# Performance work log

Hardware: AMD Instinct MI355X
Metric: run time of the kernel (lower is better)

## Reference

```python
import jax, jax.numpy as jnp
import numpy as np

H = 128          # hidden_dim
N_LAYERS = 3
N_GRAPHS = 256
LN_EPS = 1e-5


def setup_inputs() -> dict:
    key = jax.random.key(0)
    ks = jax.random.split(key, 12)
    N, E = 100000, 600000
    x = jax.random.normal(ks[0], (N, 66), dtype=jnp.float32)
    edge_index = jax.random.randint(ks[1], (2, E), 0, N, dtype=jnp.int32)
    edge_attr = jax.random.normal(ks[2], (E, 6), dtype=jnp.float32)
    batch = jnp.sort(jax.random.randint(ks[3], (N,), 0, N_GRAPHS, dtype=jnp.int32))
    # params (stored as [in, out] so y = x @ W + b)
    def lin(k, fan_in, fan_out):
        s = 1.0 / np.sqrt(fan_in)
        kw, kb = jax.random.split(k)
        return (jax.random.uniform(kw, (fan_in, fan_out), jnp.float32, -s, s),
                jax.random.uniform(kb, (fan_out,), jnp.float32, -s, s))
    w_node, b_node = lin(ks[4], 66, H)
    w_edge, b_edge = lin(ks[5], 6, H)
    mp_ws, mp_bs = [], []
    for i in range(N_LAYERS):
        w, b = lin(ks[6 + i], 3 * H, H)
        mp_ws.append(w); mp_bs.append(b)
    w_out, b_out = lin(ks[9], H, H)
    return {
        "x": x, "edge_index": edge_index, "edge_attr": edge_attr, "batch": batch,
        "w_node": w_node, "b_node": b_node, "w_edge": w_edge, "b_edge": b_edge,
        "mp_w": jnp.stack(mp_ws), "mp_b": jnp.stack(mp_bs),
        "ln_g": jnp.ones((H,), jnp.float32), "ln_b": jnp.zeros((H,), jnp.float32),
        "w_out": w_out, "b_out": b_out,
    }


def _layer_norm(h, g, b):
    mu = h.mean(-1, keepdims=True)
    var = ((h - mu) ** 2).mean(-1, keepdims=True)
    return (h - mu) * jax.lax.rsqrt(var + LN_EPS) * g + b


def reference(x, edge_index, edge_attr, batch, w_node, b_node, w_edge, b_edge,
              mp_w, mp_b, ln_g, ln_b, w_out, b_out):
    h = x @ w_node + b_node                      # [N, H]
    ef = edge_attr @ w_edge + b_edge             # [E, H]
    src, dst = edge_index[0], edge_index[1]
    for i in range(N_LAYERS):
        W = mp_w[i]                               # [3H, H], split to avoid concat
        Ws, Wd, We = W[:H], W[H:2 * H], W[2 * H:]
        # per-edge message = Linear(concat(h[src], h[dst], ef)); original takes a
        # GLOBAL mean over all edges -> single [H] vector broadcast to all nodes
        msgs = h[src] @ Ws + h[dst] @ Wd + ef @ We   # [E, H]
        mean_msg = msgs.mean(axis=0) + mp_b[i]       # [H]
        h = h + mean_msg
        h = jax.nn.relu(_layer_norm(h, ln_g, ln_b))
        # dropout is identity in eval mode
    counts = jax.ops.segment_sum(jnp.ones((h.shape[0],), h.dtype), batch,
                                 num_segments=N_GRAPHS)
    pooled = jax.ops.segment_sum(h, batch, num_segments=N_GRAPHS)
    pooled = pooled / jnp.maximum(counts, 1.0)[:, None]   # global_mean_pool
    return pooled @ w_out + b_out                 # [N_GRAPHS, H]
```

## Files before the change

### kernel.cpp

```cpp
#include <hip/hip_runtime.h>

#define HDIM 128
#define XDIM 66
#define EDIM 6
#define NGRAPHS 256
#define LN_EPS 1e-5f
#define T0ROWS 64

#define HBINS 25600
#define HR 4
#define HB 32
#define CBINS (HR * HBINS)
#define NBX 1024

__global__ __launch_bounds__(256) void k_hist_part(const int* __restrict__ ei,
        float* __restrict__ part, int E) {
    __shared__ float lh[HBINS];
    int b = blockIdx.x;
    int s = b & (HB - 1);
    int r = (b / HB) & (HR - 1);
    int a = b / (HB * HR);
    int t = threadIdx.x;
    for (int i = t; i < HBINS; i += 256) lh[i] = 0.f;
    __syncthreads();
    const int* src = ei + (size_t)a * E;
    int chunk = (((E + HB - 1) / HB) + 3) & ~3;
    int lo = s * chunk;
    int hi = min(E, lo + chunk);
    int base = r * HBINS;
    if ((E & 3) == 0) {
        for (int i = lo + t * 4; i < hi; i += 256 * 4) {
            if (i + 4 <= hi) {
                int4 v = *(const int4*)(src + i);
                unsigned u0 = (unsigned)(v.x - base);
                unsigned u1 = (unsigned)(v.y - base);
                unsigned u2 = (unsigned)(v.z - base);
                unsigned u3 = (unsigned)(v.w - base);
                if (u0 < HBINS) atomicAdd(&lh[u0], 1.0f);
                if (u1 < HBINS) atomicAdd(&lh[u1], 1.0f);
                if (u2 < HBINS) atomicAdd(&lh[u2], 1.0f);
                if (u3 < HBINS) atomicAdd(&lh[u3], 1.0f);
            } else {
                for (int j = i; j < hi; ++j) {
                    unsigned u = (unsigned)(src[j] - base);
                    if (u < HBINS) atomicAdd(&lh[u], 1.0f);
                }
            }
        }
    } else {
        for (int i = lo + t; i < hi; i += 256) {
            unsigned u = (unsigned)(src[i] - base);
            if (u < HBINS) atomicAdd(&lh[u], 1.0f);
        }
    }
    __syncthreads();
    float* dst = part + (size_t)b * HBINS;
    for (int i = t; i < HBINS / 4; i += 256)
        ((float4*)dst)[i] = ((const float4*)lh)[i];
}

__global__ __launch_bounds__(256) void k_hist_red(const float* __restrict__ part,
        float* __restrict__ c_src, float* __restrict__ c_dst) {
    int n = blockIdx.x * 256 + threadIdx.x;
    if (n >= CBINS) return;
    int r = n / HBINS, off = n - r * HBINS;
    const float* p0 = part + ((size_t)(0 * HR + r) * HB) * HBINS + off;
    const float* p1 = part + ((size_t)(1 * HR + r) * HB) * HBINS + off;
    float s0 = 0.f, s1 = 0.f;
#pragma unroll 8
    for (int s = 0; s < HB; ++s) {
        s0 += p0[(size_t)s * HBINS];
        s1 += p1[(size_t)s * HBINS];
    }
    c_src[n] = s0;
    c_dst[n] = s1;
}

__global__ __launch_bounds__(256) void k_edgesum(const float* __restrict__ ea,
                                                 float* __restrict__ sum_attr, int E) {
    int nchunk = E >> 1;
    float a0 = 0, a1 = 0, a2 = 0, a3 = 0, a4 = 0, a5 = 0;
    for (int c = blockIdx.x * blockDim.x + threadIdx.x; c < nchunk;
         c += gridDim.x * blockDim.x) {
        const float4* p = (const float4*)(ea + (size_t)c * 12);
        float4 v0 = p[0], v1 = p[1], v2 = p[2];
        a0 += v0.x + v1.z;  a1 += v0.y + v1.w;  a2 += v0.z + v2.x;
        a3 += v0.w + v2.y;  a4 += v1.x + v2.z;  a5 += v1.y + v2.w;
    }
#pragma unroll
    for (int m = 32; m; m >>= 1) {
        a0 += __shfl_xor(a0, m); a1 += __shfl_xor(a1, m); a2 += __shfl_xor(a2, m);
        a3 += __shfl_xor(a3, m); a4 += __shfl_xor(a4, m); a5 += __shfl_xor(a5, m);
    }
    __shared__ float sbuf[4][6];
    int lane = threadIdx.x & 63, w = threadIdx.x >> 6;
    if (lane == 0) {
        sbuf[w][0] = a0; sbuf[w][1] = a1; sbuf[w][2] = a2;
        sbuf[w][3] = a3; sbuf[w][4] = a4; sbuf[w][5] = a5;
    }
    __syncthreads();
    if (threadIdx.x < 6) {
        float s = sbuf[0][threadIdx.x] + sbuf[1][threadIdx.x] +
                  sbuf[2][threadIdx.x] + sbuf[3][threadIdx.x];
        atomicAdd(&sum_attr[threadIdx.x], s);
    }
    if (blockIdx.x == 0 && threadIdx.x < 6 && (E & 1))
        atomicAdd(&sum_attr[threadIdx.x], ea[(size_t)(E - 1) * 6 + threadIdx.x]);
}

__global__ __launch_bounds__(256) void k_xsum(const float* __restrict__ x,
        const float* __restrict__ c_src, const float* __restrict__ c_dst,
        float* __restrict__ xpart, int N) {
    int lane = threadIdx.x & 63, w = threadIdx.x >> 6;
    int wid = blockIdx.x * 4 + w, nw = gridDim.x * 4;
    float as0 = 0, ad0 = 0, as1 = 0, ad1 = 0;
    int Q = N >> 2;
    for (int q = wid; q < Q; q += nw) {
        int n = q * 4;
        const float* xr = x + (size_t)n * XDIM;
        float x0 = xr[lane];
        float x1 = xr[XDIM + lane];
        float x2 = xr[2 * XDIM + lane];
        float x3 = xr[3 * XDIM + lane];
        float4 cs = *(const float4*)(c_src + n);
        float4 cd = *(const float4*)(c_dst + n);
        as0 = fmaf(cs.x, x0, as0); as0 = fmaf(cs.y, x1, as0);
        as0 = fmaf(cs.z, x2, as0); as0 = fmaf(cs.w, x3, as0);
        ad0 = fmaf(cd.x, x0, ad0); ad0 = fmaf(cd.y, x1, ad0);
        ad0 = fmaf(cd.z, x2, ad0); ad0 = fmaf(cd.w, x3, ad0);
        if (lane < 2) {
            float e0 = xr[64 + lane];
            float e1 = xr[XDIM + 64 + lane];
            float e2 = xr[2 * XDIM + 64 + lane];
            float e3 = xr[3 * XDIM + 64 + lane];
            as1 = fmaf(cs.x, e0, as1); as1 = fmaf(cs.y, e1, as1);
            as1 = fmaf(cs.z, e2, as1); as1 = fmaf(cs.w, e3, as1);
            ad1 = fmaf(cd.x, e0, ad1); ad1 = fmaf(cd.y, e1, ad1);
            ad1 = fmaf(cd.z, e2, ad1); ad1 = fmaf(cd.w, e3, ad1);
        }
    }
    if (wid == 0) {
        for (int n = Q * 4; n < N; ++n) {
            const float* xr = x + (size_t)n * XDIM;
            float cs = c_src[n], cd = c_dst[n];
            float xv = xr[lane];
            as0 = fmaf(cs, xv, as0);
            ad0 = fmaf(cd, xv, ad0);
            if (lane < 2) {
                float xe = xr[64 + lane];
                as1 = fmaf(cs, xe, as1);
                ad1 = fmaf(cd, xe, ad1);
            }
        }
    }
    __shared__ float redS[4][XDIM], redD[4][XDIM];
    redS[w][lane] = as0;  redD[w][lane] = ad0;
    if (lane < 2) { redS[w][64 + lane] = as1;  redD[w][64 + lane] = ad1; }
    __syncthreads();
    int t = threadIdx.x;
    float* xp = xpart + (size_t)blockIdx.x * 136;
    if (t < XDIM) {
        xp[t]        = redS[0][t] + redS[1][t] + redS[2][t] + redS[3][t];
        xp[XDIM + t] = redD[0][t] + redD[1][t] + redD[2][t] + redD[3][t];
    }
}

__global__ __launch_bounds__(64) void k_xred(const float* __restrict__ xpart,
                                             float* __restrict__ xs, int nb) {
    int e = blockIdx.x;
    int lane = threadIdx.x;
    float s = 0.f;
    for (int b = lane; b < nb; b += 64)
        s += xpart[(size_t)b * 136 + e];
#pragma unroll
    for (int m = 32; m; m >>= 1) s += __shfl_xor(s, m);
    if (lane == 0) xs[e] = s;
}

template <int FIRST>
__global__ __launch_bounds__(256) void k_mm(const float* __restrict__ sv,
        const float* __restrict__ sum_attr, const float* __restrict__ w_edge,
        const float* __restrict__ b_edge, const float* __restrict__ W,
        const float* __restrict__ mpb, float* __restrict__ mean_msg, float Ef,
        const float* __restrict__ w_node, const float* __restrict__ b_node) {
    __shared__ float sc[384];
    __shared__ float mred[256];
    int t = threadIdx.x;
    if (t < 128) {
        float ssrc, sdst;
        if (FIRST) {
            ssrc = Ef * b_node[t];
            sdst = ssrc;
#pragma unroll
            for (int k = 0; k < XDIM; ++k) {
                float wv = w_node[k * HDIM + t];
                ssrc = fmaf(sv[k], wv, ssrc);
                sdst = fmaf(sv[XDIM + k], wv, sdst);
            }
        } else {
            ssrc = sv[t] + sv[t + 128];
            sdst = sv[256 + t] + sv[384 + t];
        }
        sc[t] = ssrc;
        sc[128 + t] = sdst;
        float se = Ef * b_edge[t];
#pragma unroll
        for (int k = 0; k < EDIM; ++k) se = fmaf(sum_attr[k], w_edge[k * HDIM + t], se);
        sc[256 + t] = se;
    }
    __syncthreads();
    int col = blockIdx.x * 16 + (t & 15);
    int rg = t >> 4;
    float acc = 0.f;
#pragma unroll 4
    for (int r = rg * 24; r < rg * 24 + 24; ++r)
        acc = fmaf(sc[r], W[r * HDIM + col], acc);
    mred[t] = acc;
    __syncthreads();
    if (t < 16) {
        float s = 0.f;
#pragma unroll
        for (int g = 0; g < 16; ++g) s += mred[g * 16 + t];
        mean_msg[blockIdx.x * 16 + t] = s / Ef + mpb[blockIdx.x * 16 + t];
    }
}

__global__ __launch_bounds__(256) void k_red(const float* __restrict__ partials,
                                             float* __restrict__ sbuf, int nb) {
    int b0 = blockIdx.x * 32;
    int b1 = min(nb, b0 + 32);
    int t = threadIdx.x;
    float s0 = 0.f, s1 = 0.f;
    for (int b = b0; b < b1; ++b) {
        const float* row = partials + (size_t)b * 512;
        s0 += row[t];
        s1 += row[t + 256];
    }
    atomicAdd(&sbuf[t], s0);
    atomicAdd(&sbuf[t + 256], s1);
}

__global__ __launch_bounds__(256) void k_upd0(
        const float* __restrict__ x, const float* __restrict__ w_node,
        const float* __restrict__ b_node, const float* __restrict__ mean_msg,
        const float* __restrict__ ln_g, const float* __restrict__ ln_b,
        const float* __restrict__ c_src, const float* __restrict__ c_dst,
        float* __restrict__ h, float* __restrict__ partials, int N, int ntiles) {
    __shared__ float wl[XDIM * HDIM];
    __shared__ float xl[T0ROWS * XDIM];
    int t = threadIdx.x;
    int cg = t & 31, rg = t >> 5;
    int c0 = cg * 4;
    for (int i = t; i < XDIM * HDIM / 2; i += 256)
        ((float2*)wl)[i] = ((const float2*)w_node)[i];
    float4 b4 = *(const float4*)(b_node + c0);
    float4 m4 = *(const float4*)(mean_msg + c0);
    float4 bm = {b4.x + m4.x, b4.y + m4.y, b4.z + m4.z, b4.w + m4.w};
    float4 g4  = *(const float4*)(ln_g + c0);
    float4 lb4 = *(const float4*)(ln_b + c0);
    float4 accS = {0, 0, 0, 0}, accD = {0, 0, 0, 0};

    for (int tile = blockIdx.x; tile < ntiles; tile += gridDim.x) {
        int rowbase = tile * T0ROWS;
        const float* xg = x + (size_t)rowbase * XDIM;
        int vr = min(T0ROWS, N - rowbase);
        int lim = vr * XDIM;
        __syncthreads();
        for (int i = t; i < T0ROWS * XDIM / 2; i += 256) {
            int e = i * 2;
            float2 vv;
            if (e + 2 <= lim) vv = *(const float2*)(xg + e);
            else { vv.x = (e < lim) ? xg[e] : 0.f; vv.y = (e + 1 < lim) ? xg[e + 1] : 0.f; }
            ((float2*)xl)[i] = vv;
        }
        __syncthreads();

        float4 acc[8];
#pragma unroll
        for (int j = 0; j < 8; ++j) acc[j] = bm;
        const float* xrow = xl + rg * 8 * XDIM;
#pragma unroll 6
        for (int k = 0; k < XDIM; ++k) {
            float4 wv = *(const float4*)(wl + k * HDIM + c0);
#pragma unroll
            for (int j = 0; j < 8; ++j) {
                float xv = xrow[j * XDIM + k];
                acc[j].x = fmaf(xv, wv.x, acc[j].x);
                acc[j].y = fmaf(xv, wv.y, acc[j].y);
                acc[j].z = fmaf(xv, wv.z, acc[j].z);
                acc[j].w = fmaf(xv, wv.w, acc[j].w);
            }
        }
        float4 csA = *(const float4*)(c_src + rowbase + rg * 8);
        float4 csB = *(const float4*)(c_src + rowbase + rg * 8 + 4);
        float4 cdA = *(const float4*)(c_dst + rowbase + rg * 8);
        float4 cdB = *(const float4*)(c_dst + rowbase + rg * 8 + 4);
        float csArr[8] = {csA.x, csA.y, csA.z, csA.w, csB.x, csB.y, csB.z, csB.w};
        float cdArr[8] = {cdA.x, cdA.y, cdA.z, cdA.w, cdB.x, cdB.y, cdB.z, cdB.w};
#pragma unroll
        for (int j = 0; j < 8; ++j) {
            float4 a = acc[j];
            float s = a.x + a.y + a.z + a.w;
#pragma unroll
            for (int m = 16; m; m >>= 1) s += __shfl_xor(s, m);
            float mu = s * (1.0f / HDIM);
            float d0 = a.x - mu, d1 = a.y - mu, d2 = a.z - mu, d3 = a.w - mu;
            float q = d0 * d0 + d1 * d1 + d2 * d2 + d3 * d3;
#pragma unroll
            for (int m = 16; m; m >>= 1) q += __shfl_xor(q, m);
            float rs = rsqrtf(q * (1.0f / HDIM) + LN_EPS);
            float4 o;
            o.x = fmaxf(0.f, fmaf(d0 * rs, g4.x, lb4.x));
            o.y = fmaxf(0.f, fmaf(d1 * rs, g4.y, lb4.y));
            o.z = fmaxf(0.f, fmaf(d2 * rs, g4.z, lb4.z));
            o.w = fmaxf(0.f, fmaf(d3 * rs, g4.w, lb4.w));
            int row = rowbase + rg * 8 + j;
            if (row < N)
                *(float4*)(h + (size_t)row * HDIM + c0) = o;
            float cs = csArr[j], cd = cdArr[j];
            accS.x = fmaf(cs, o.x, accS.x); accS.y = fmaf(cs, o.y, accS.y);
            accS.z = fmaf(cs, o.z, accS.z); accS.w = fmaf(cs, o.w, accS.w);
            accD.x = fmaf(cd, o.x, accD.x); accD.y = fmaf(cd, o.y, accD.y);
            accD.z = fmaf(cd, o.z, accD.z); accD.w = fmaf(cd, o.w, accD.w);
        }
    }
    __syncthreads();
    float* red = xl;
    *(float4*)(red + rg * HDIM + c0) = accS;
    *(float4*)(red + 1024 + rg * HDIM + c0) = accD;
    __syncthreads();
    if (t < 128) {
        float s = 0.f, d = 0.f;
#pragma unroll
        for (int gi = 0; gi < 8; ++gi) {
            s += red[gi * HDIM + t];
            d += red[1024 + gi * HDIM + t];
        }
        float* row = partials + (size_t)blockIdx.x * 512;
        row[t] = s;        row[t + 128] = 0.f;
        row[t + 256] = d;  row[t + 384] = 0.f;
    }
}

__device__ __forceinline__ float2 ln_relu2(float2 v, float2 g, float2 bb) {
    float s = v.x + v.y;
#pragma unroll
    for (int m = 32; m; m >>= 1) s += __shfl_xor(s, m);
    float mu = s * (1.0f / HDIM);
    float dx = v.x - mu, dy = v.y - mu;
    float q = dx * dx + dy * dy;
#pragma unroll
    for (int m = 32; m; m >>= 1) q += __shfl_xor(q, m);
    float rs = rsqrtf(q * (1.0f / HDIM) + LN_EPS);
    float2 o;
    o.x = fmaxf(0.f, fmaf(dx * rs, g.x, bb.x));
    o.y = fmaxf(0.f, fmaf(dy * rs, g.y, bb.y));
    return o;
}

template <int LAST>
__global__ __launch_bounds__(256) void k_update(
        float* __restrict__ h, const float* __restrict__ mean_msg,
        const float* __restrict__ ln_g, const float* __restrict__ ln_b,
        const float* __restrict__ c_src, const float* __restrict__ c_dst,
        const int* __restrict__ batch, float* __restrict__ partials,
        float* __restrict__ pooled, int N, int cpb) {
    int t = threadIdx.x;
    int lane = t & 63, w = t >> 6;
    int c0 = lane * 2;
    float2 mm = *(const float2*)(mean_msg + c0);
    float2 g  = *(const float2*)(ln_g + c0);
    float2 bb = *(const float2*)(ln_b + c0);
    int start = blockIdx.x * cpb;
    int end = min(N, start + cpb);
    int spw = (cpb + 3) >> 2;
    int ns = start + w * spw;
    int ne = min(end, ns + spw);
    float2 accS = {0.f, 0.f}, accD = {0.f, 0.f}, accP = {0.f, 0.f};
    int cur_g = -1;
    int n = ns;
    for (; n + 4 <= ne; n += 4) {
        float2 v0 = *(const float2*)(h + (size_t)(n    ) * HDIM + c0);
        float2 v1 = *(const float2*)(h + (size_t)(n + 1) * HDIM + c0);
        float2 v2 = *(const float2*)(h + (size_t)(n + 2) * HDIM + c0);
        float2 v3 = *(const float2*)(h + (size_t)(n + 3) * HDIM + c0);
        v0.x += mm.x; v0.y += mm.y;  v1.x += mm.x; v1.y += mm.y;
        v2.x += mm.x; v2.y += mm.y;  v3.x += mm.x; v3.y += mm.y;
        float2 o0 = ln_relu2(v0, g, bb);
        float2 o1 = ln_relu2(v1, g, bb);
        float2 o2 = ln_relu2(v2, g, bb);
        float2 o3 = ln_relu2(v3, g, bb);
        if (LAST) {
            int gi[4] = {batch[n], batch[n + 1], batch[n + 2], batch[n + 3]};
            float2 oo[4] = {o0, o1, o2, o3};
#pragma unroll
            for (int r = 0; r < 4; ++r) {
                if (gi[r] != cur_g) {
                    if (cur_g >= 0) {
                        atomicAdd(&pooled[cur_g * HDIM + c0],     accP.x);
                        atomicAdd(&pooled[cur_g * HDIM + c0 + 1], accP.y);
                    }
                    accP.x = 0.f; accP.y = 0.f;
                    cur_g = gi[r];
                }
                accP.x += oo[r].x; accP.y += oo[r].y;
            }
        } else {
            *(float2*)(h + (size_t)(n    ) * HDIM + c0) = o0;
            *(float2*)(h + (size_t)(n + 1) * HDIM + c0) = o1;
            *(float2*)(h + (size_t)(n + 2) * HDIM + c0) = o2;
            *(float2*)(h + (size_t)(n + 3) * HDIM + c0) = o3;
            float cs0 = c_src[n], cs1 = c_src[n+1], cs2 = c_src[n+2], cs3 = c_src[n+3];
            float cd0 = c_dst[n], cd1 = c_dst[n+1], cd2 = c_dst[n+2], cd3 = c_dst[n+3];
            accS.x = fmaf(cs0, o0.x, accS.x); accS.y = fmaf(cs0, o0.y, accS.y);
            accS.x = fmaf(cs1, o1.x, accS.x); accS.y = fmaf(cs1, o1.y, accS.y);
            accS.x = fmaf(cs2, o2.x, accS.x); accS.y = fmaf(cs2, o2.y, accS.y);
            accS.x = fmaf(cs3, o3.x, accS.x); accS.y = fmaf(cs3, o3.y, accS.y);
            accD.x = fmaf(cd0, o0.x, accD.x); accD.y = fmaf(cd0, o0.y, accD.y);
            accD.x = fmaf(cd1, o1.x, accD.x); accD.y = fmaf(cd1, o1.y, accD.y);
            accD.x = fmaf(cd2, o2.x, accD.x); accD.y = fmaf(cd2, o2.y, accD.y);
            accD.x = fmaf(cd3, o3.x, accD.x); accD.y = fmaf(cd3, o3.y, accD.y);
        }
    }
    for (; n < ne; ++n) {
        float2 v = *(const float2*)(h + (size_t)n * HDIM + c0);
        v.x += mm.x; v.y += mm.y;
        float2 o = ln_relu2(v, g, bb);
        if (LAST) {
            int gg = batch[n];
            if (gg != cur_g) {
                if (cur_g >= 0) {
                    atomicAdd(&pooled[cur_g * HDIM + c0],     accP.x);
                    atomicAdd(&pooled[cur_g * HDIM + c0 + 1], accP.y);
                }
                accP.x = 0.f; accP.y = 0.f;
                cur_g = gg;
            }
            accP.x += o.x; accP.y += o.y;
        } else {
            *(float2*)(h + (size_t)n * HDIM + c0) = o;
            float cs = c_src[n], cd = c_dst[n];
            accS.x = fmaf(cs, o.x, accS.x); accS.y = fmaf(cs, o.y, accS.y);
            accD.x = fmaf(cd, o.x, accD.x); accD.y = fmaf(cd, o.y, accD.y);
        }
    }
    if (LAST) {
        if (cur_g >= 0) {
            atomicAdd(&pooled[cur_g * HDIM + c0],     accP.x);
            atomicAdd(&pooled[cur_g * HDIM + c0 + 1], accP.y);
        }
    } else {
        __shared__ float sb[HDIM], db[HDIM];
        if (t < HDIM) { sb[t] = 0.f; db[t] = 0.f; }
        __syncthreads();
        atomicAdd(&sb[c0], accS.x); atomicAdd(&sb[c0 + 1], accS.y);
        atomicAdd(&db[c0], accD.x); atomicAdd(&db[c0 + 1], accD.y);
        __syncthreads();
        float* row = partials + (size_t)blockIdx.x * 512;
        if (t < 128) {
            row[t] = sb[t];        row[t + 128] = 0.f;
            row[t + 256] = db[t];  row[t + 384] = 0.f;
        }
    }
}

__global__ __launch_bounds__(128) void k_out(const float* __restrict__ pooled,
        const int* __restrict__ batch, const float* __restrict__ w_out,
        const float* __restrict__ b_out, float* __restrict__ out, int N) {
    int gph = blockIdx.x;
    int t = threadIdx.x;
    __shared__ float p[HDIM];
    __shared__ int cntS;
    if (t == 0) {
        int lo = 0, hi = N;
        while (lo < hi) { int mid = (lo + hi) >> 1; if (batch[mid] < gph) lo = mid + 1; else hi = mid; }
        int lo2 = lo, hi2 = N;
        while (lo2 < hi2) { int mid = (lo2 + hi2) >> 1; if (batch[mid] <= gph) lo2 = mid + 1; else hi2 = mid; }
        cntS = lo2 - lo;
    }
    __syncthreads();
    float inv = 1.0f / fmaxf((float)cntS, 1.0f);
    p[t] = pooled[gph * HDIM + t] * inv;
    __syncthreads();
    float acc = b_out[t];
#pragma unroll 8
    for (int k = 0; k < HDIM; ++k) acc = fmaf(p[k], w_out[k * HDIM + t], acc);
    out[gph * HDIM + t] = acc;
}

extern "C" void kernel_launch(void* const* d_in, const int* in_sizes, int n_in,
                              void* d_out, int out_size, void* d_ws, size_t ws_size,
                              hipStream_t stream) {
    const float* x      = (const float*)d_in[0];
    const int*   ei     = (const int*)d_in[1];
    const float* ea     = (const float*)d_in[2];
    const int*   batch  = (const int*)d_in[3];
    const float* w_node = (const float*)d_in[4];
    const float* b_node = (const float*)d_in[5];
    const float* w_edge = (const float*)d_in[6];
    const float* b_edge = (const float*)d_in[7];
    const float* mp_w   = (const float*)d_in[8];
    const float* mp_b   = (const float*)d_in[9];
    const float* ln_g   = (const float*)d_in[10];
    const float* ln_b   = (const float*)d_in[11];
    const float* w_out  = (const float*)d_in[12];
    const float* b_out  = (const float*)d_in[13];
    float* out = (float*)d_out;
    int N = in_sizes[3];
    int E = in_sizes[2] / EDIM;
    float Ef = (float)E;
    int ntiles = (N + T0ROWS - 1) / T0ROWS;

    float* ws = (float*)d_ws;
    size_t off = 0;
    float* h        = ws + off; off += (size_t)N * HDIM;
    float* hist_part = h;
    float* partials = ws + off; off += (size_t)1024 * 512;
    float* mean_msg = ws + off; off += 128;
    float* c_src    = ws + off; off += CBINS;
    float* c_dst    = ws + off; off += CBINS;
    float* xpart    = ws + off; off += (size_t)NBX * 136;
    float* xs       = ws + off; off += 136;
    float* acc0     = ws + off;
    float* sum_attr = ws + off; off += 8;
    float* sbuf1    = ws + off; off += 512;
    float* sbuf2    = ws + off; off += 512;
    float* pooled   = ws + off; off += NGRAPHS * HDIM;
    size_t zero_count = (size_t)(ws + off - acc0);
    hipMemsetAsync(acc0, 0, zero_count * sizeof(float), stream);

    k_hist_part<<<2 * HR * HB, 256, 0, stream>>>(ei, hist_part, E);
    k_hist_red<<<(CBINS + 255) / 256, 256, 0, stream>>>(hist_part, c_src, c_dst);
    k_edgesum<<<128, 256, 0, stream>>>(ea, sum_attr, E);
    k_xsum<<<NBX, 256, 0, stream>>>(x, c_src, c_dst, xpart, N);
    k_xred<<<2 * XDIM, 64, 0, stream>>>(xpart, xs, NBX);

    const int NB0 = 768;
    const int NB = 1024;
    int cpb = (N + NB - 1) / NB;

    k_mm<1><<<8, 256, 0, stream>>>(xs, sum_attr, w_edge, b_edge,
                                   mp_w, mp_b, mean_msg, Ef, w_node, b_node);
    k_upd0<<<NB0, 256, 0, stream>>>(x, w_node, b_node, mean_msg, ln_g, ln_b,
                                    c_src, c_dst, h, partials, N, ntiles);
    k_red<<<(NB0 + 31) / 32, 256, 0, stream>>>(partials, sbuf1, NB0);
    k_mm<0><<<8, 256, 0, stream>>>(sbuf1, sum_attr, w_edge, b_edge,
                                   mp_w + (size_t)1 * 384 * HDIM,
                                   mp_b + (size_t)1 * HDIM, mean_msg, Ef,
                                   w_node, b_node);
    k_update<0><<<NB, 256, 0, stream>>>(h, mean_msg, ln_g, ln_b, c_src, c_dst,
                                        batch, partials, pooled, N, cpb);
    k_red<<<NB / 32, 256, 0, stream>>>(partials, sbuf2, NB);
    k_mm<0><<<8, 256, 0, stream>>>(sbuf2, sum_attr, w_edge, b_edge,
                                   mp_w + (size_t)2 * 384 * HDIM,
                                   mp_b + (size_t)2 * HDIM, mean_msg, Ef,
                                   w_node, b_node);
    k_update<1><<<NB, 256, 0, stream>>>(h, mean_msg, ln_g, ln_b, c_src, c_dst,
                                        batch, partials, pooled, N, cpb);

    k_out<<<NGRAPHS, HDIM, 0, stream>>>(pooled, batch, w_out, b_out, out, N);
}
```

Baseline: 178.7 us.

## Retile first node-embedding update with 8x8 register blocking and one tile per block

```diff
diff --git a/kernel.cpp b/kernel.cpp
--- a/kernel.cpp
+++ b/kernel.cpp
@@ -5,13 +5,15 @@
 #define EDIM 6
 #define NGRAPHS 256
 #define LN_EPS 1e-5f
-#define T0ROWS 64
 
 #define HBINS 25600
 #define HR 4
-#define HB 32
+#define HB 16
 #define CBINS (HR * HBINS)
 #define NBX 1024
+
+#define T0R 64
+#define T0PAD 532
 
 __global__ __launch_bounds__(256) void k_hist_part(const int* __restrict__ ei,
         float* __restrict__ part, int E) {
@@ -240,106 +242,127 @@
     atomicAdd(&sbuf[t + 256], s1);
 }
 
-__global__ __launch_bounds__(256) void k_upd0(
+__global__ __launch_bounds__(128) void k_upd0(
         const float* __restrict__ x, const float* __restrict__ w_node,
         const float* __restrict__ b_node, const float* __restrict__ mean_msg,
         const float* __restrict__ ln_g, const float* __restrict__ ln_b,
         const float* __restrict__ c_src, const float* __restrict__ c_dst,
-        float* __restrict__ h, float* __restrict__ partials, int N, int ntiles) {
-    __shared__ float wl[XDIM * HDIM];
-    __shared__ float xl[T0ROWS * XDIM];
-    int t = threadIdx.x;
-    int cg = t & 31, rg = t >> 5;
-    int c0 = cg * 4;
-    for (int i = t; i < XDIM * HDIM / 2; i += 256)
-        ((float2*)wl)[i] = ((const float2*)w_node)[i];
-    float4 b4 = *(const float4*)(b_node + c0);
-    float4 m4 = *(const float4*)(mean_msg + c0);
-    float4 bm = {b4.x + m4.x, b4.y + m4.y, b4.z + m4.z, b4.w + m4.w};
-    float4 g4  = *(const float4*)(ln_g + c0);
-    float4 lb4 = *(const float4*)(ln_b + c0);
-    float4 accS = {0, 0, 0, 0}, accD = {0, 0, 0, 0};
-
-    for (int tile = blockIdx.x; tile < ntiles; tile += gridDim.x) {
-        int rowbase = tile * T0ROWS;
-        const float* xg = x + (size_t)rowbase * XDIM;
-        int vr = min(T0ROWS, N - rowbase);
-        int lim = vr * XDIM;
-        __syncthreads();
-        for (int i = t; i < T0ROWS * XDIM / 2; i += 256) {
-            int e = i * 2;
-            float2 vv;
-            if (e + 2 <= lim) vv = *(const float2*)(xg + e);
-            else { vv.x = (e < lim) ? xg[e] : 0.f; vv.y = (e + 1 < lim) ? xg[e + 1] : 0.f; }
-            ((float2*)xl)[i] = vv;
-        }
-        __syncthreads();
-
-        float4 acc[8];
-#pragma unroll
-        for (int j = 0; j < 8; ++j) acc[j] = bm;
-        const float* xrow = xl + rg * 8 * XDIM;
-#pragma unroll 6
-        for (int k = 0; k < XDIM; ++k) {
-            float4 wv = *(const float4*)(wl + k * HDIM + c0);
-#pragma unroll
-            for (int j = 0; j < 8; ++j) {
-                float xv = xrow[j * XDIM + k];
-                acc[j].x = fmaf(xv, wv.x, acc[j].x);
-                acc[j].y = fmaf(xv, wv.y, acc[j].y);
-                acc[j].z = fmaf(xv, wv.z, acc[j].z);
-                acc[j].w = fmaf(xv, wv.w, acc[j].w);
-            }
-        }
-        float4 csA = *(const float4*)(c_src + rowbase + rg * 8);
-        float4 csB = *(const float4*)(c_src + rowbase + rg * 8 + 4);
-        float4 cdA = *(const float4*)(c_dst + rowbase + rg * 8);
-        float4 cdB = *(const float4*)(c_dst + rowbase + rg * 8 + 4);
-        float csArr[8] = {csA.x, csA.y, csA.z, csA.w, csB.x, csB.y, csB.z, csB.w};
-        float cdArr[8] = {cdA.x, cdA.y, cdA.z, cdA.w, cdB.x, cdB.y, cdB.z, cdB.w};
-#pragma unroll
-        for (int j = 0; j < 8; ++j) {
-            float4 a = acc[j];
-            float s = a.x + a.y + a.z + a.w;
-#pragma unroll
-            for (int m = 16; m; m >>= 1) s += __shfl_xor(s, m);
-            float mu = s * (1.0f / HDIM);
-            float d0 = a.x - mu, d1 = a.y - mu, d2 = a.z - mu, d3 = a.w - mu;
-            float q = d0 * d0 + d1 * d1 + d2 * d2 + d3 * d3;
-#pragma unroll
-            for (int m = 16; m; m >>= 1) q += __shfl_xor(q, m);
-            float rs = rsqrtf(q * (1.0f / HDIM) + LN_EPS);
-            float4 o;
-            o.x = fmaxf(0.f, fmaf(d0 * rs, g4.x, lb4.x));
-            o.y = fmaxf(0.f, fmaf(d1 * rs, g4.y, lb4.y));
-            o.z = fmaxf(0.f, fmaf(d2 * rs, g4.z, lb4.z));
-            o.w = fmaxf(0.f, fmaf(d3 * rs, g4.w, lb4.w));
-            int row = rowbase + rg * 8 + j;
-            if (row < N)
-                *(float4*)(h + (size_t)row * HDIM + c0) = o;
-            float cs = csArr[j], cd = cdArr[j];
-            accS.x = fmaf(cs, o.x, accS.x); accS.y = fmaf(cs, o.y, accS.y);
-            accS.z = fmaf(cs, o.z, accS.z); accS.w = fmaf(cs, o.w, accS.w);
-            accD.x = fmaf(cd, o.x, accD.x); accD.y = fmaf(cd, o.y, accD.y);
-            accD.z = fmaf(cd, o.z, accD.z); accD.w = fmaf(cd, o.w, accD.w);
-        }
-    }
-    __syncthreads();
-    float* red = xl;
-    *(float4*)(red + rg * HDIM + c0) = accS;
-    *(float4*)(red + 1024 + rg * HDIM + c0) = accD;
-    __syncthreads();
-    if (t < 128) {
-        float s = 0.f, d = 0.f;
-#pragma unroll
-        for (int gi = 0; gi < 8; ++gi) {
-            s += red[gi * HDIM + t];
-            d += red[1024 + gi * HDIM + t];
-        }
-        float* row = partials + (size_t)blockIdx.x * 512;
-        row[t] = s;        row[t + 128] = 0.f;
-        row[t + 256] = d;  row[t + 384] = 0.f;
-    }
+        float* __restrict__ h, float* __restrict__ partials, int N) {
+    __shared__ float wl[16 * T0PAD];
+    __shared__ float xt[8 * T0PAD];
+    int t = threadIdx.x;
+    int cg = t & 15, rg = t >> 4;
+    for (int i = t; i < XDIM * HDIM; i += 128) {
+        int k = i >> 7, c = i & 127;
+        wl[(c >> 3) * T0PAD + k * 8 + (c & 7)] = w_node[i];
+    }
+    int rowbase = blockIdx.x * T0R;
+    const float* xg = x + (size_t)rowbase * XDIM;
+    int lim = (min(T0R, N - rowbase)) * XDIM;
+    for (int i = t; i < T0R * XDIM; i += 128) {
+        float v = (i < lim) ? xg[i] : 0.f;
+        int r = i / XDIM, k = i - r * XDIM;
+        xt[(r >> 3) * T0PAD + k * 8 + (r & 7)] = v;
+    }
+    int c0 = cg * 8;
+    float4 b4a = *(const float4*)(b_node + c0);
+    float4 b4b = *(const float4*)(b_node + c0 + 4);
+    float4 m4a = *(const float4*)(mean_msg + c0);
+    float4 m4b = *(const float4*)(mean_msg + c0 + 4);
+    float4 bma = {b4a.x + m4a.x, b4a.y + m4a.y, b4a.z + m4a.z, b4a.w + m4a.w};
+    float4 bmb = {b4b.x + m4b.x, b4b.y + m4b.y, b4b.z + m4b.z, b4b.w + m4b.w};
+    float4 ga  = *(const float4*)(ln_g + c0);
+    float4 gb  = *(const float4*)(ln_g + c0 + 4);
+    float4 lba = *(const float4*)(ln_b + c0);
+    float4 lbb = *(const float4*)(ln_b + c0 + 4);
+    __syncthreads();
+
+    float4 acc[8][2];
+#pragma unroll
+    for (int r = 0; r < 8; ++r) { acc[r][0] = bma; acc[r][1] = bmb; }
+    const float* xp = xt + rg * T0PAD;
+    const float* wp = wl + cg * T0PAD;
+#pragma unroll 2
+    for (int k = 0; k < XDIM; ++k) {
+        float4 xa = *(const float4*)(xp + k * 8);
+        float4 xb = *(const float4*)(xp + k * 8 + 4);
+        float4 wa = *(const float4*)(wp + k * 8);
+        float4 wb = *(const float4*)(wp + k * 8 + 4);
+        float xr[8] = {xa.x, xa.y, xa.z, xa.w, xb.x, xb.y, xb.z, xb.w};
+#pragma unroll
+        for (int r = 0; r < 8; ++r) {
+            acc[r][0].x = fmaf(xr[r], wa.x, acc[r][0].x);
+            acc[r][0].y = fmaf(xr[r], wa.y, acc[r][0].y);
+            acc[r][0].z = fmaf(xr[r], wa.z, acc[r][0].z);
+            acc[r][0].w = fmaf(xr[r], wa.w, acc[r][0].w);
+            acc[r][1].x = fmaf(xr[r], wb.x, acc[r][1].x);
+            acc[r][1].y = fmaf(xr[r], wb.y, acc[r][1].y);
+            acc[r][1].z = fmaf(xr[r], wb.z, acc[r][1].z);
+            acc[r][1].w = fmaf(xr[r], wb.w, acc[r][1].w);
+        }
+    }
+    int rbase = rowbase + rg * 8;
+    float4 csA = *(const float4*)(c_src + rbase);
+    float4 csB = *(const float4*)(c_src + rbase + 4);
+    float4 cdA = *(const float4*)(c_dst + rbase);
+    float4 cdB = *(const float4*)(c_dst + rbase + 4);
+    float csArr[8] = {csA.x, csA.y, csA.z, csA.w, csB.x, csB.y, csB.z, csB.w};
+    float cdArr[8] = {cdA.x, cdA.y, cdA.z, cdA.w, cdB.x, cdB.y, cdB.z, cdB.w};
+    float4 accS0 = {0,0,0,0}, accS1 = {0,0,0,0}, accD0 = {0,0,0,0}, accD1 = {0,0,0,0};
+#pragma unroll
+    for (int r = 0; r < 8; ++r) {
+        float4 a0 = acc[r][0], a1 = acc[r][1];
+        float s = a0.x + a0.y + a0.z + a0.w + a1.x + a1.y + a1.z + a1.w;
+#pragma unroll
+        for (int m = 8; m; m >>= 1) s += __shfl_xor(s, m);
+        float mu = s * (1.0f / HDIM);
+        float d0 = a0.x - mu, d1 = a0.y - mu, d2 = a0.z - mu, d3 = a0.w - mu;
+        float d4 = a1.x - mu, d5 = a1.y - mu, d6 = a1.z - mu, d7 = a1.w - mu;
+        float q = d0*d0 + d1*d1 + d2*d2 + d3*d3 + d4*d4 + d5*d5 + d6*d6 + d7*d7;
+#pragma unroll
+        for (int m = 8; m; m >>= 1) q += __shfl_xor(q, m);
+        float rs = rsqrtf(q * (1.0f / HDIM) + LN_EPS);
+        float4 o0, o1;
+        o0.x = fmaxf(0.f, fmaf(d0 * rs, ga.x, lba.x));
+        o0.y = fmaxf(0.f, fmaf(d1 * rs, ga.y, lba.y));
+        o0.z = fmaxf(0.f, fmaf(d2 * rs, ga.z, lba.z));
+        o0.w = fmaxf(0.f, fmaf(d3 * rs, ga.w, lba.w));
+        o1.x = fmaxf(0.f, fmaf(d4 * rs, gb.x, lbb.x));
+        o1.y = fmaxf(0.f, fmaf(d5 * rs, gb.y, lbb.y));
+        o1.z = fmaxf(0.f, fmaf(d6 * rs, gb.z, lbb.z));
+        o1.w = fmaxf(0.f, fmaf(d7 * rs, gb.w, lbb.w));
+        int row = rbase + r;
+        if (row < N) {
+            *(float4*)(h + (size_t)row * HDIM + c0) = o0;
+            *(float4*)(h + (size_t)row * HDIM + c0 + 4) = o1;
+        }
+        float cs = csArr[r], cd = cdArr[r];
+        accS0.x = fmaf(cs, o0.x, accS0.x); accS0.y = fmaf(cs, o0.y, accS0.y);
+        accS0.z = fmaf(cs, o0.z, accS0.z); accS0.w = fmaf(cs, o0.w, accS0.w);
+        accS1.x = fmaf(cs, o1.x, accS1.x); accS1.y = fmaf(cs, o1.y, accS1.y);
+        accS1.z = fmaf(cs, o1.z, accS1.z); accS1.w = fmaf(cs, o1.w, accS1.w);
+        accD0.x = fmaf(cd, o0.x, accD0.x); accD0.y = fmaf(cd, o0.y, accD0.y);
+        accD0.z = fmaf(cd, o0.z, accD0.z); accD0.w = fmaf(cd, o0.w, accD0.w);
+        accD1.x = fmaf(cd, o1.x, accD1.x); accD1.y = fmaf(cd, o1.y, accD1.y);
+        accD1.z = fmaf(cd, o1.z, accD1.z); accD1.w = fmaf(cd, o1.w, accD1.w);
+    }
+    __syncthreads();
+    float* redS = xt;
+    float* redD = xt + 1024;
+    *(float4*)(redS + rg * HDIM + c0)     = accS0;
+    *(float4*)(redS + rg * HDIM + c0 + 4) = accS1;
+    *(float4*)(redD + rg * HDIM + c0)     = accD0;
+    *(float4*)(redD + rg * HDIM + c0 + 4) = accD1;
+    __syncthreads();
+    float s = 0.f, d = 0.f;
+#pragma unroll
+    for (int gi = 0; gi < 8; ++gi) {
+        s += redS[gi * HDIM + t];
+        d += redD[gi * HDIM + t];
+    }
+    float* row = partials + (size_t)blockIdx.x * 512;
+    row[t] = s;        row[t + 128] = 0.f;
+    row[t + 256] = d;  row[t + 384] = 0.f;
 }
 
 __device__ __forceinline__ float2 ln_relu2(float2 v, float2 g, float2 bb) {
@@ -509,13 +532,13 @@
     int N = in_sizes[3];
     int E = in_sizes[2] / EDIM;
     float Ef = (float)E;
-    int ntiles = (N + T0ROWS - 1) / T0ROWS;
+    int ntiles0 = (N + T0R - 1) / T0R;
 
     float* ws = (float*)d_ws;
     size_t off = 0;
     float* h        = ws + off; off += (size_t)N * HDIM;
     float* hist_part = h;
-    float* partials = ws + off; off += (size_t)1024 * 512;
+    float* partials = ws + off; off += (size_t)2048 * 512;
     float* mean_msg = ws + off; off += 128;
     float* c_src    = ws + off; off += CBINS;
     float* c_dst    = ws + off; off += CBINS;
@@ -535,15 +558,14 @@
     k_xsum<<<NBX, 256, 0, stream>>>(x, c_src, c_dst, xpart, N);
     k_xred<<<2 * XDIM, 64, 0, stream>>>(xpart, xs, NBX);
 
-    const int NB0 = 768;
     const int NB = 1024;
     int cpb = (N + NB - 1) / NB;
 
     k_mm<1><<<8, 256, 0, stream>>>(xs, sum_attr, w_edge, b_edge,
                                    mp_w, mp_b, mean_msg, Ef, w_node, b_node);
-    k_upd0<<<NB0, 256, 0, stream>>>(x, w_node, b_node, mean_msg, ln_g, ln_b,
-                                    c_src, c_dst, h, partials, N, ntiles);
-    k_red<<<(NB0 + 31) / 32, 256, 0, stream>>>(partials, sbuf1, NB0);
+    k_upd0<<<ntiles0, 128, 0, stream>>>(x, w_node, b_node, mean_msg, ln_g, ln_b,
+                                        c_src, c_dst, h, partials, N);
+    k_red<<<(ntiles0 + 31) / 32, 256, 0, stream>>>(partials, sbuf1, ntiles0);
     k_mm<0><<<8, 256, 0, stream>>>(sbuf1, sum_attr, w_edge, b_edge,
                                    mp_w + (size_t)1 * 384 * HDIM,
                                    mp_b + (size_t)1 * HDIM, mean_msg, Ef,
```

Result: slower. 207.6 us (+16.2%).

## Compute first-layer node projection with bf16 MFMA and one tile per block

Applied to the files above, without the earlier changes.

```diff
diff --git a/kernel.cpp b/kernel.cpp
--- a/kernel.cpp
+++ b/kernel.cpp
@@ -5,13 +5,32 @@
 #define EDIM 6
 #define NGRAPHS 256
 #define LN_EPS 1e-5f
-#define T0ROWS 64
 
 #define HBINS 25600
 #define HR 4
-#define HB 32
+#define HB 16
 #define CBINS (HR * HBINS)
 #define NBX 1024
+
+#define KP 104
+
+typedef __attribute__((ext_vector_type(8))) short sv8;
+typedef __attribute__((ext_vector_type(4))) float fv4;
+
+__device__ __forceinline__ unsigned short f2bf(float f) {
+    unsigned u = __float_as_uint(f);
+    unsigned r = (u + 0x7FFFu + ((u >> 16) & 1u)) >> 16;
+    return (unsigned short)r;
+}
+
+__global__ __launch_bounds__(128) void k_prep(const float* __restrict__ w_node,
+                                              unsigned short* __restrict__ wtg) {
+    int col = threadIdx.x;
+    for (int kp = 0; kp < KP; ++kp) {
+        float v = (kp < XDIM) ? w_node[kp * HDIM + col] : 0.f;
+        wtg[col * KP + kp] = f2bf(v);
+    }
+}
 
 __global__ __launch_bounds__(256) void k_hist_part(const int* __restrict__ ei,
         float* __restrict__ part, int E) {
@@ -241,104 +260,129 @@
 }
 
 __global__ __launch_bounds__(256) void k_upd0(
-        const float* __restrict__ x, const float* __restrict__ w_node,
+        const float* __restrict__ x, const unsigned short* __restrict__ wtg,
         const float* __restrict__ b_node, const float* __restrict__ mean_msg,
         const float* __restrict__ ln_g, const float* __restrict__ ln_b,
         const float* __restrict__ c_src, const float* __restrict__ c_dst,
-        float* __restrict__ h, float* __restrict__ partials, int N, int ntiles) {
-    __shared__ float wl[XDIM * HDIM];
-    __shared__ float xl[T0ROWS * XDIM];
+        float* __restrict__ h, float* __restrict__ partials, int N) {
+    __shared__ unsigned short xl[64 * KP];
+    __shared__ unsigned short wt[128 * KP];
     int t = threadIdx.x;
-    int cg = t & 31, rg = t >> 5;
-    int c0 = cg * 4;
-    for (int i = t; i < XDIM * HDIM / 2; i += 256)
-        ((float2*)wl)[i] = ((const float2*)w_node)[i];
-    float4 b4 = *(const float4*)(b_node + c0);
-    float4 m4 = *(const float4*)(mean_msg + c0);
-    float4 bm = {b4.x + m4.x, b4.y + m4.y, b4.z + m4.z, b4.w + m4.w};
-    float4 g4  = *(const float4*)(ln_g + c0);
-    float4 lb4 = *(const float4*)(ln_b + c0);
-    float4 accS = {0, 0, 0, 0}, accD = {0, 0, 0, 0};
-
-    for (int tile = blockIdx.x; tile < ntiles; tile += gridDim.x) {
-        int rowbase = tile * T0ROWS;
-        const float* xg = x + (size_t)rowbase * XDIM;
-        int vr = min(T0ROWS, N - rowbase);
-        int lim = vr * XDIM;
-        __syncthreads();
-        for (int i = t; i < T0ROWS * XDIM / 2; i += 256) {
-            int e = i * 2;
-            float2 vv;
-            if (e + 2 <= lim) vv = *(const float2*)(xg + e);
-            else { vv.x = (e < lim) ? xg[e] : 0.f; vv.y = (e + 1 < lim) ? xg[e + 1] : 0.f; }
-            ((float2*)xl)[i] = vv;
-        }
-        __syncthreads();
-
-        float4 acc[8];
-#pragma unroll
-        for (int j = 0; j < 8; ++j) acc[j] = bm;
-        const float* xrow = xl + rg * 8 * XDIM;
-#pragma unroll 6
-        for (int k = 0; k < XDIM; ++k) {
-            float4 wv = *(const float4*)(wl + k * HDIM + c0);
-#pragma unroll
-            for (int j = 0; j < 8; ++j) {
-                float xv = xrow[j * XDIM + k];
-                acc[j].x = fmaf(xv, wv.x, acc[j].x);
-                acc[j].y = fmaf(xv, wv.y, acc[j].y);
-                acc[j].z = fmaf(xv, wv.z, acc[j].z);
-                acc[j].w = fmaf(xv, wv.w, acc[j].w);
-            }
-        }
-        float4 csA = *(const float4*)(c_src + rowbase + rg * 8);
-        float4 csB = *(const float4*)(c_src + rowbase + rg * 8 + 4);
-        float4 cdA = *(const float4*)(c_dst + rowbase + rg * 8);
-        float4 cdB = *(const float4*)(c_dst + rowbase + rg * 8 + 4);
-        float csArr[8] = {csA.x, csA.y, csA.z, csA.w, csB.x, csB.y, csB.z, csB.w};
-        float cdArr[8] = {cdA.x, cdA.y, cdA.z, cdA.w, cdB.x, cdB.y, cdB.z, cdB.w};
-#pragma unroll
-        for (int j = 0; j < 8; ++j) {
-            float4 a = acc[j];
-            float s = a.x + a.y + a.z + a.w;
-#pragma unroll
-            for (int m = 16; m; m >>= 1) s += __shfl_xor(s, m);
-            float mu = s * (1.0f / HDIM);
-            float d0 = a.x - mu, d1 = a.y - mu, d2 = a.z - mu, d3 = a.w - mu;
-            float q = d0 * d0 + d1 * d1 + d2 * d2 + d3 * d3;
-#pragma unroll
-            for (int m = 16; m; m >>= 1) q += __shfl_xor(q, m);
-            float rs = rsqrtf(q * (1.0f / HDIM) + LN_EPS);
-            float4 o;
-            o.x = fmaxf(0.f, fmaf(d0 * rs, g4.x, lb4.x));
-            o.y = fmaxf(0.f, fmaf(d1 * rs, g4.y, lb4.y));
-            o.z = fmaxf(0.f, fmaf(d2 * rs, g4.z, lb4.z));
-            o.w = fmaxf(0.f, fmaf(d3 * rs, g4.w, lb4.w));
-            int row = rowbase + rg * 8 + j;
-            if (row < N)
-                *(float4*)(h + (size_t)row * HDIM + c0) = o;
-            float cs = csArr[j], cd = cdArr[j];
-            accS.x = fmaf(cs, o.x, accS.x); accS.y = fmaf(cs, o.y, accS.y);
-            accS.z = fmaf(cs, o.z, accS.z); accS.w = fmaf(cs, o.w, accS.w);
-            accD.x = fmaf(cd, o.x, accD.x); accD.y = fmaf(cd, o.y, accD.y);
-            accD.z = fmaf(cd, o.z, accD.z); accD.w = fmaf(cd, o.w, accD.w);
-        }
-    }
-    __syncthreads();
-    float* red = xl;
-    *(float4*)(red + rg * HDIM + c0) = accS;
-    *(float4*)(red + 1024 + rg * HDIM + c0) = accD;
+    int lane = t & 63, w = t >> 6;
+    {
+        const uint4* srcp = (const uint4*)wtg;
+        uint4* dstp = (uint4*)wt;
+        for (int i = t; i < 128 * KP / 8; i += 256) dstp[i] = srcp[i];
+    }
+    for (int i = t; i < 64 * KP / 2; i += 256) ((unsigned*)xl)[i] = 0u;
+    __syncthreads();
+    int rowbase = blockIdx.x * 64;
+    const float* xg = x + (size_t)rowbase * XDIM;
+    int lim = min(64, N - rowbase) * XDIM;
+    for (int i = t; i < 64 * XDIM; i += 256) {
+        if (i < lim) {
+            int r = i / XDIM, k = i - r * XDIM;
+            xl[r * KP + k] = f2bf(xg[i]);
+        }
+    }
+    int cl = lane & 15, g = lane >> 4;
+    float bm[8], gg[8], lb[8];
+#pragma unroll
+    for (int ct = 0; ct < 8; ++ct) {
+        int col = ct * 16 + cl;
+        bm[ct] = b_node[col] + mean_msg[col];
+        gg[ct] = ln_g[col];
+        lb[ct] = ln_b[col];
+    }
+    __syncthreads();
+
+    fv4 acc[8];
+#pragma unroll
+    for (int ct = 0; ct < 8; ++ct) acc[ct] = (fv4){0.f, 0.f, 0.f, 0.f};
+#pragma unroll
+    for (int ks = 0; ks < 3; ++ks) {
+        sv8 a = *(const sv8*)&xl[(w * 16 + cl) * KP + ks * 32 + g * 8];
+#pragma unroll
+        for (int ct = 0; ct < 8; ++ct) {
+            sv8 b = *(const sv8*)&wt[(ct * 16 + cl) * KP + ks * 32 + g * 8];
+            acc[ct] = __builtin_amdgcn_mfma_f32_16x16x32_bf16(a, b, acc[ct], 0, 0, 0);
+        }
+    }
+    float v[8][4];
+    float s[4] = {0.f, 0.f, 0.f, 0.f};
+#pragma unroll
+    for (int ct = 0; ct < 8; ++ct)
+#pragma unroll
+        for (int e = 0; e < 4; ++e) {
+            v[ct][e] = acc[ct][e] + bm[ct];
+            s[e] += v[ct][e];
+        }
+#pragma unroll
+    for (int m = 1; m < 16; m <<= 1) {
+        s[0] += __shfl_xor(s[0], m); s[1] += __shfl_xor(s[1], m);
+        s[2] += __shfl_xor(s[2], m); s[3] += __shfl_xor(s[3], m);
+    }
+    float mu[4], q[4] = {0.f, 0.f, 0.f, 0.f};
+#pragma unroll
+    for (int e = 0; e < 4; ++e) mu[e] = s[e] * (1.0f / HDIM);
+#pragma unroll
+    for (int ct = 0; ct < 8; ++ct)
+#pragma unroll
+        for (int e = 0; e < 4; ++e) {
+            float d = v[ct][e] - mu[e];
+            q[e] = fmaf(d, d, q[e]);
+        }
+#pragma unroll
+    for (int m = 1; m < 16; m <<= 1) {
+        q[0] += __shfl_xor(q[0], m); q[1] += __shfl_xor(q[1], m);
+        q[2] += __shfl_xor(q[2], m); q[3] += __shfl_xor(q[3], m);
+    }
+    float rs[4];
+#pragma unroll
+    for (int e = 0; e < 4; ++e) rs[e] = rsqrtf(q[e] * (1.0f / HDIM) + LN_EPS);
+
+    int grow = rowbase + w * 16 + g * 4;
+    float4 csv = *(const float4*)(c_src + grow);
+    float4 cdv = *(const float4*)(c_dst + grow);
+    float cs[4] = {csv.x, csv.y, csv.z, csv.w};
+    float cd[4] = {cdv.x, cdv.y, cdv.z, cdv.w};
+    float accS[8], accD[8];
+#pragma unroll
+    for (int ct = 0; ct < 8; ++ct) { accS[ct] = 0.f; accD[ct] = 0.f; }
+#pragma unroll
+    for (int e = 0; e < 4; ++e) {
+        int row = grow + e;
+        bool ok = (row < N);
+#pragma unroll
+        for (int ct = 0; ct < 8; ++ct) {
+            float o = fmaxf(0.f, fmaf((v[ct][e] - mu[e]) * rs[e], gg[ct], lb[ct]));
+            if (ok) h[(size_t)row * HDIM + ct * 16 + cl] = o;
+            accS[ct] = fmaf(cs[e], o, accS[ct]);
+            accD[ct] = fmaf(cd[e], o, accD[ct]);
+        }
+    }
+#pragma unroll
+    for (int ct = 0; ct < 8; ++ct) {
+        accS[ct] += __shfl_xor(accS[ct], 16); accS[ct] += __shfl_xor(accS[ct], 32);
+        accD[ct] += __shfl_xor(accD[ct], 16); accD[ct] += __shfl_xor(accD[ct], 32);
+    }
+    __syncthreads();
+    float* redS = (float*)xl;
+    float* redD = redS + 512;
+    if (g == 0) {
+#pragma unroll
+        for (int ct = 0; ct < 8; ++ct) {
+            redS[w * HDIM + ct * 16 + cl] = accS[ct];
+            redD[w * HDIM + ct * 16 + cl] = accD[ct];
+        }
+    }
     __syncthreads();
     if (t < 128) {
-        float s = 0.f, d = 0.f;
-#pragma unroll
-        for (int gi = 0; gi < 8; ++gi) {
-            s += red[gi * HDIM + t];
-            d += red[1024 + gi * HDIM + t];
-        }
+        float ss = redS[t] + redS[128 + t] + redS[256 + t] + redS[384 + t];
+        float dd = redD[t] + redD[128 + t] + redD[256 + t] + redD[384 + t];
         float* row = partials + (size_t)blockIdx.x * 512;
-        row[t] = s;        row[t + 128] = 0.f;
-        row[t + 256] = d;  row[t + 384] = 0.f;
+        row[t] = ss;       row[t + 128] = 0.f;
+        row[t + 256] = dd; row[t + 384] = 0.f;
     }
 }
 
@@ -509,18 +553,20 @@
     int N = in_sizes[3];
     int E = in_sizes[2] / EDIM;
     float Ef = (float)E;
-    int ntiles = (N + T0ROWS - 1) / T0ROWS;
+    int ntiles0 = (N + 63) / 64;
 
     float* ws = (float*)d_ws;
     size_t off = 0;
     float* h        = ws + off; off += (size_t)N * HDIM;
     float* hist_part = h;
-    float* partials = ws + off; off += (size_t)1024 * 512;
+    float* partials = ws + off; off += (size_t)2048 * 512;
     float* mean_msg = ws + off; off += 128;
     float* c_src    = ws + off; off += CBINS;
     float* c_dst    = ws + off; off += CBINS;
     float* xpart    = ws + off; off += (size_t)NBX * 136;
+    unsigned short* wtg = (unsigned short*)(ws + off); off += 128 * KP / 2;
     float* xs       = ws + off; off += 136;
+    off = (off + 3) & ~(size_t)3;
     float* acc0     = ws + off;
     float* sum_attr = ws + off; off += 8;
     float* sbuf1    = ws + off; off += 512;
@@ -529,21 +575,21 @@
     size_t zero_count = (size_t)(ws + off - acc0);
     hipMemsetAsync(acc0, 0, zero_count * sizeof(float), stream);
 
+    k_prep<<<1, 128, 0, stream>>>(w_node, wtg);
     k_hist_part<<<2 * HR * HB, 256, 0, stream>>>(ei, hist_part, E);
     k_hist_red<<<(CBINS + 255) / 256, 256, 0, stream>>>(hist_part, c_src, c_dst);
     k_edgesum<<<128, 256, 0, stream>>>(ea, sum_attr, E);
     k_xsum<<<NBX, 256, 0, stream>>>(x, c_src, c_dst, xpart, N);
     k_xred<<<2 * XDIM, 64, 0, stream>>>(xpart, xs, NBX);
 
-    const int NB0 = 768;
     const int NB = 1024;
     int cpb = (N + NB - 1) / NB;
 
     k_mm<1><<<8, 256, 0, stream>>>(xs, sum_attr, w_edge, b_edge,
                                    mp_w, mp_b, mean_msg, Ef, w_node, b_node);
-    k_upd0<<<NB0, 256, 0, stream>>>(x, w_node, b_node, mean_msg, ln_g, ln_b,
-                                    c_src, c_dst, h, partials, N, ntiles);
-    k_red<<<(NB0 + 31) / 32, 256, 0, stream>>>(partials, sbuf1, NB0);
+    k_upd0<<<ntiles0, 256, 0, stream>>>(x, wtg, b_node, mean_msg, ln_g, ln_b,
+                                        c_src, c_dst, h, partials, N);
+    k_red<<<(ntiles0 + 31) / 32, 256, 0, stream>>>(partials, sbuf1, ntiles0);
     k_mm<0><<<8, 256, 0, stream>>>(sbuf1, sum_attr, w_edge, b_edge,
                                    mp_w + (size_t)1 * 384 * HDIM,
                                    mp_b + (size_t)1 * HDIM, mean_msg, Ef,
```

Result: slower. 195.1 us (+9.2%).
